# Kernel optimization log

Hardware: AMD Instinct MI355X
Metric: run time of the kernel (lower is better)

The kernel has to match this reference:

```python
import jax, jax.numpy as jnp
import numpy as np

EPS = 1e-5

def setup_inputs() -> dict:
    key = jax.random.key(0)
    k1, k2, k3, k4, k5 = jax.random.split(key, 5)
    B, N, K, HW, C = 2, 128, 64, 65536, 134
    # class probabilities (rows need not be normalized for the matcher math)
    input_class_prob = jax.random.uniform(k1, (B, N, C), dtype=jnp.float32)
    # predicted mask probabilities in [0, 1]
    input_mask = jax.random.uniform(k2, (B, N, HW), dtype=jnp.float32)
    # binary ground-truth masks (stored as float32 for the reduction math)
    target_mask = (jax.random.uniform(k3, (B, K, HW)) > 0.7).astype(jnp.float32)
    target_class = jax.random.randint(k4, (B, K), 0, C, dtype=jnp.int64)
    target_sizes = jax.random.randint(k5, (B,), 1, K + 1, dtype=jnp.int64)
    return {
        "input_class_prob": input_class_prob,
        "input_mask": input_mask,
        "target_mask": target_mask,
        "target_class": target_class,
        "target_sizes": target_sizes,
    }


def reference(input_class_prob, input_mask, target_mask, target_class, target_sizes):
    """Similarity-matrix stage of HungarianMatcher.

    Returns sim: (B, N, K) = sim_class * sim_dice.
    The subsequent scipy linear_sum_assignment is CPU-only with
    data-dependent shapes and is excluded from the kernelizable math.
    """
    B, N, _ = input_class_prob.shape
    K = target_class.shape[-1]
    # sim_class[b, n, k] = input_class_prob[b, n, target_class[b, k]]
    idx = jnp.broadcast_to(target_class[:, None, :], (B, N, K))
    sim_class = jnp.take_along_axis(input_class_prob, idx, axis=-1)
    # dice similarity without materializing the (B, N, K, HW) broadcast:
    # intersections via GEMM, cardinalities via row/col sums + broadcast.
    intersections = jnp.einsum("bnp,bkp->bnk", input_mask, target_mask)
    cardinalities = input_mask.sum(-1)[:, :, None] + target_mask.sum(-1)[:, None, :]
    sim_dice = (2.0 * intersections + EPS) / (cardinalities + EPS)
    return sim_class * sim_dice
```

## Files before the change

### kernel.cpp

```cpp
#include <hip/hip_runtime.h>

#define HWX 65536
#define NQ 128
#define KT 64
#define CC 134
#define BB 2
#define NW 256
#define WIN 256
#define SUB 64
#define NSUB 4
#define EPSI 1e-5f

typedef __attribute__((ext_vector_type(4))) float f32x4;
typedef __attribute__((ext_vector_type(8))) short bf16x8;
typedef __attribute__((ext_vector_type(2))) unsigned int u32x2;

static __device__ __forceinline__ unsigned int cvtpk(float lo, float hi) {
  unsigned int r;
  asm("v_cvt_pk_bf16_f32 %0, %1, %2" : "=v"(r) : "v"(lo), "v"(hi));
  return r;
}

__global__ void hm_detect(const unsigned int* __restrict__ t,
                          unsigned int* __restrict__ flag) {
  unsigned int w = t[threadIdx.x * 2 + 1];
  unsigned long long any = __ballot(w != 0u);
  if (threadIdx.x == 0) *flag = (any != 0ull) ? 1u : 0u;
}

template <bool ATOMIC>
__global__ __launch_bounds__(512, 4)
void hm_stage1(const float* __restrict__ in_mask, const float* __restrict__ tg_mask,
               float* __restrict__ Ipart, float* __restrict__ RSin,
               float* __restrict__ RStg) {
  const int w = blockIdx.x & (NW - 1);
  const int b = blockIdx.x >> 8;
  const int tid = threadIdx.x;
  const int lane = tid & 63;
  const int wv = tid >> 6;
  const int srow = tid >> 4;
  const int c4 = (tid & 15) * 4;
  const int c8b = (tid & 15) * 8;
  const int l16 = lane & 15;
  const int lg = lane >> 4;

  __shared__ unsigned short lA[2][128 * 64];
  __shared__ unsigned short lB[2][64 * 64];

  const float* Ab = in_mask + (size_t)b * NQ * HWX + (size_t)w * WIN;
  const float* Bb = tg_mask + (size_t)b * KT * HWX + (size_t)w * WIN;

  f32x4 ra4[4], rb4[2];
  f32x4 acc[4];
  #pragma unroll
  for (int i = 0; i < 4; ++i) acc[i] = f32x4{0.f, 0.f, 0.f, 0.f};
  float rsA[4] = {0.f, 0.f, 0.f, 0.f};
  float rsB[2] = {0.f, 0.f};

  auto ISSUE = [&](int t) {
    const int co = t * SUB + c4;
    #pragma unroll
    for (int it = 0; it < 4; ++it)
      ra4[it] = *(const f32x4*)(Ab + (size_t)(it * 32 + srow) * HWX + co);
    #pragma unroll
    for (int it = 0; it < 2; ++it)
      rb4[it] = *(const f32x4*)(Bb + (size_t)(it * 32 + srow) * HWX + co);
  };

  auto CVTW = [&](int buf) {
    char* A8 = (char*)lA[buf];
    char* B8 = (char*)lB[buf];
    #pragma unroll
    for (int it = 0; it < 4; ++it) {
      f32x4 x = ra4[it];
      rsA[it] += (x.x + x.y) + (x.z + x.w);
      u32x2 v;
      v.x = cvtpk(x.x, x.y); v.y = cvtpk(x.z, x.w);
      const int row = it * 32 + srow;
      *(u32x2*)(A8 + ((row * 128 + c8b) ^ ((row & 7) << 4))) = v;
    }
    #pragma unroll
    for (int it = 0; it < 2; ++it) {
      f32x4 x = rb4[it];
      rsB[it] += (x.x + x.y) + (x.z + x.w);
      u32x2 v;
      v.x = cvtpk(x.x, x.y); v.y = cvtpk(x.z, x.w);
      const int row = it * 32 + srow;
      *(u32x2*)(B8 + ((row * 128 + c8b) ^ ((row & 7) << 4))) = v;
    }
  };

  auto COMP = [&](int buf) {
    const char* A8 = (const char*)lA[buf];
    const char* B8 = (const char*)lB[buf];
    const int arow = wv * 16 + l16;
    const int sw = (l16 & 7) << 4;
    #pragma unroll
    for (int s = 0; s < 2; ++s) {
      bf16x8 fa = *(const bf16x8*)(A8 + ((arow * 128 + s * 64 + lg * 16) ^ sw));
      #pragma unroll
      for (int cf = 0; cf < 4; ++cf) {
        const int brow = cf * 16 + l16;
        bf16x8 fb = *(const bf16x8*)(B8 + ((brow * 128 + s * 64 + lg * 16) ^ sw));
        acc[cf] = __builtin_amdgcn_mfma_f32_16x16x32_bf16(fa, fb, acc[cf], 0, 0, 0);
      }
    }
  };

  ISSUE(0);
  CVTW(0);
  __syncthreads();
  #pragma unroll
  for (int t = 0; t < NSUB; ++t) {
    if (t + 1 < NSUB) ISSUE(t + 1);
    COMP(t & 1);
    if (t + 1 < NSUB) {
      CVTW((t + 1) & 1);
      __syncthreads();
    }
  }

  #pragma unroll
  for (int cf = 0; cf < 4; ++cf) {
    #pragma unroll
    for (int j = 0; j < 4; ++j) {
      const int row = wv * 16 + lg * 4 + j;
      const int col = cf * 16 + l16;
      if (!ATOMIC)
        Ipart[((size_t)(b * NW + w) * NQ + row) * KT + col] = acc[cf][j];
      else
        atomicAdd(&Ipart[((size_t)b * NQ + row) * KT + col], acc[cf][j]);
    }
  }

  #pragma unroll
  for (int it = 0; it < 4; ++it) {
    float v = rsA[it];
    v += __shfl_xor(v, 1); v += __shfl_xor(v, 2);
    v += __shfl_xor(v, 4); v += __shfl_xor(v, 8);
    rsA[it] = v;
  }
  #pragma unroll
  for (int it = 0; it < 2; ++it) {
    float v = rsB[it];
    v += __shfl_xor(v, 1); v += __shfl_xor(v, 2);
    v += __shfl_xor(v, 4); v += __shfl_xor(v, 8);
    rsB[it] = v;
  }
  if ((tid & 15) == 0) {
    if (!ATOMIC) {
      #pragma unroll
      for (int it = 0; it < 4; ++it)
        RSin[(size_t)(b * NW + w) * NQ + it * 32 + srow] = rsA[it];
      #pragma unroll
      for (int it = 0; it < 2; ++it)
        RStg[(size_t)(b * NW + w) * KT + it * 32 + srow] = rsB[it];
    } else {
      #pragma unroll
      for (int it = 0; it < 4; ++it)
        atomicAdd(&RSin[b * NQ + it * 32 + srow], rsA[it]);
      #pragma unroll
      for (int it = 0; it < 2; ++it)
        atomicAdd(&RStg[b * KT + it * 32 + srow], rsB[it]);
    }
  }
}

__global__ __launch_bounds__(256)
void hm_stage2(const float* __restrict__ cprob, const void* __restrict__ tcls,
               const float* __restrict__ Ipart, const float* __restrict__ RSin,
               const float* __restrict__ RStg, float* __restrict__ out) {
  const int bn = blockIdx.x;
  const int b = bn >> 7, n = bn & 127;
  const int k = threadIdx.x & 63;
  const int wq = threadIdx.x >> 6;
  float I = 0.f, ra = 0.f, rg = 0.f;
  #pragma unroll 8
  for (int ww = 0; ww < NW / 4; ++ww) {
    const int w = wq * (NW / 4) + ww;
    I  += Ipart[((size_t)(b * NW + w) * NQ + n) * KT + k];
    ra += RSin[(size_t)(b * NW + w) * NQ + n];
    rg += RStg[(size_t)(b * NW + w) * KT + k];
  }
  __shared__ float sI[4][64];
  __shared__ float sG[4][64];
  __shared__ float sR[4];
  sI[wq][k] = I;
  sG[wq][k] = rg;
  if (k == 0) sR[wq] = ra;
  __syncthreads();
  if (wq == 0) {
    I  = sI[0][k] + sI[1][k] + sI[2][k] + sI[3][k];
    rg = sG[0][k] + sG[1][k] + sG[2][k] + sG[3][k];
    ra = sR[0] + sR[1] + sR[2] + sR[3];
    const unsigned int hiw = ((const unsigned int*)tcls)[k * 2 + 1];
    const bool i32 = (__ballot(hiw != 0u) != 0ull);
    int tc = i32 ? ((const int*)tcls)[b * KT + k]
                 : (int)((const long long*)tcls)[b * KT + k];
    const float c = cprob[((size_t)b * NQ + n) * CC + tc];
    out[(size_t)bn * KT + k] = c * (2.f * I + EPSI) / (ra + rg + EPSI);
  }
}

__global__ __launch_bounds__(256)
void hm_stage2_direct(const float* __restrict__ cprob, const void* __restrict__ tcls,
                      const unsigned int* __restrict__ flag,
                      const float* __restrict__ Iacc, const float* __restrict__ RSin,
                      const float* __restrict__ RStg, float* __restrict__ out) {
  const int idx = blockIdx.x * 256 + threadIdx.x;
  const int k = idx & 63;
  const int n = (idx >> 6) & 127;
  const int b = idx >> 13;
  const float I  = Iacc[idx];
  const float ra = RSin[b * NQ + n];
  const float rg = RStg[b * KT + k];
  int tc;
  if (*flag) tc = ((const int*)tcls)[b * KT + k];
  else       tc = (int)((const long long*)tcls)[b * KT + k];
  const float c = cprob[((size_t)b * NQ + n) * CC + tc];
  out[idx] = c * (2.f * I + EPSI) / (ra + rg + EPSI);
}

__global__ void hm_zero(float* __restrict__ p, int n) {
  int i = blockIdx.x * blockDim.x + threadIdx.x;
  if (i < n) p[i] = 0.f;
}

extern "C" void kernel_launch(void* const* d_in, const int* in_sizes, int n_in,
                              void* d_out, int out_size, void* d_ws, size_t ws_size,
                              hipStream_t stream) {
  const float* cprob = (const float*)d_in[0];
  const float* imask = (const float*)d_in[1];
  const float* tmask = (const float*)d_in[2];
  const void*  tcls  = d_in[3];
  float* out = (float*)d_out;

  const size_t ipart_f = (size_t)BB * NW * NQ * KT;
  const size_t rsin_f  = (size_t)BB * NW * NQ;
  const size_t rstg_f  = (size_t)BB * NW * KT;
  const size_t need    = (ipart_f + rsin_f + rstg_f) * sizeof(float);

  char* ws = (char*)d_ws;
  if (ws_size >= need) {
    float* Ipart = (float*)ws;
    float* RSin  = Ipart + ipart_f;
    float* RStg  = RSin + rsin_f;
    hm_stage1<false><<<BB * NW, 512, 0, stream>>>(imask, tmask, Ipart, RSin, RStg);
    hm_stage2<<<BB * NQ, 256, 0, stream>>>(cprob, tcls, Ipart, RSin, RStg, out);
  } else {
    float* Iacc = (float*)ws;
    float* RSin = Iacc + (size_t)BB * NQ * KT;
    float* RStg = RSin + BB * NQ;
    unsigned int* flag = (unsigned int*)(RStg + BB * KT);
    const int zn = BB * NQ * KT + BB * NQ + BB * KT;
    hm_zero<<<(zn + 255) / 256, 256, 0, stream>>>(Iacc, zn);
    hm_detect<<<1, 64, 0, stream>>>((const unsigned int*)tcls, flag);
    hm_stage1<true><<<BB * NW, 512, 0, stream>>>(imask, tmask, Iacc, RSin, RStg);
    hm_stage2_direct<<<(BB * NQ * KT) / 256, 256, 0, stream>>>(cprob, tcls, flag, Iacc, RSin, RStg, out);
  }
}
```

Measured before the change: 29.33 us.

## Stage fp32 tiles via direct global-to-LDS loads and convert to bf16 at fragment read

```diff
diff --git a/kernel.cpp b/kernel.cpp
--- a/kernel.cpp
+++ b/kernel.cpp
@@ -5,21 +5,34 @@
 #define KT 64
 #define CC 134
 #define BB 2
-#define NW 256
-#define WIN 256
+#define NW 128
+#define WIN 512
 #define SUB 64
-#define NSUB 4
+#define NSUB 8
 #define EPSI 1e-5f
 
 typedef __attribute__((ext_vector_type(4))) float f32x4;
 typedef __attribute__((ext_vector_type(8))) short bf16x8;
-typedef __attribute__((ext_vector_type(2))) unsigned int u32x2;
+
+union FU { unsigned int u[4]; bf16x8 v; };
 
 static __device__ __forceinline__ unsigned int cvtpk(float lo, float hi) {
   unsigned int r;
   asm("v_cvt_pk_bf16_f32 %0, %1, %2" : "=v"(r) : "v"(lo), "v"(hi));
   return r;
 }
+
+static __device__ __forceinline__ void gload16(const float* g, float* l) {
+  __builtin_amdgcn_global_load_lds(
+      (const __attribute__((address_space(1))) void*)g,
+      (__attribute__((address_space(3))) void*)l, 16, 0, 0);
+}
+
+#define STAGE_SYNC()                                           \
+  do {                                                         \
+    asm volatile("s_waitcnt vmcnt(0)" ::: "memory");           \
+    __syncthreads();                                           \
+  } while (0)
 
 __global__ void hm_detect(const unsigned int* __restrict__ t,
                           unsigned int* __restrict__ flag) {
@@ -29,95 +42,83 @@
 }
 
 template <bool ATOMIC>
-__global__ __launch_bounds__(512, 4)
+__global__ __launch_bounds__(512)
 void hm_stage1(const float* __restrict__ in_mask, const float* __restrict__ tg_mask,
                float* __restrict__ Ipart, float* __restrict__ RSin,
                float* __restrict__ RStg) {
   const int w = blockIdx.x & (NW - 1);
-  const int b = blockIdx.x >> 8;
+  const int b = blockIdx.x >> 7;
   const int tid = threadIdx.x;
   const int lane = tid & 63;
   const int wv = tid >> 6;
-  const int srow = tid >> 4;
-  const int c4 = (tid & 15) * 4;
-  const int c8b = (tid & 15) * 8;
   const int l16 = lane & 15;
   const int lg = lane >> 4;
 
-  __shared__ unsigned short lA[2][128 * 64];
-  __shared__ unsigned short lB[2][64 * 64];
+  __shared__ __align__(16) float lA[2][128 * SUB];
+  __shared__ __align__(16) float lB[2][64 * SUB];
 
   const float* Ab = in_mask + (size_t)b * NQ * HWX + (size_t)w * WIN;
   const float* Bb = tg_mask + (size_t)b * KT * HWX + (size_t)w * WIN;
 
-  f32x4 ra4[4], rb4[2];
   f32x4 acc[4];
   #pragma unroll
   for (int i = 0; i < 4; ++i) acc[i] = f32x4{0.f, 0.f, 0.f, 0.f};
-  float rsA[4] = {0.f, 0.f, 0.f, 0.f};
-  float rsB[2] = {0.f, 0.f};
-
-  auto ISSUE = [&](int t) {
-    const int co = t * SUB + c4;
-    #pragma unroll
-    for (int it = 0; it < 4; ++it)
-      ra4[it] = *(const f32x4*)(Ab + (size_t)(it * 32 + srow) * HWX + co);
-    #pragma unroll
-    for (int it = 0; it < 2; ++it)
-      rb4[it] = *(const f32x4*)(Bb + (size_t)(it * 32 + srow) * HWX + co);
+  float rsA = 0.f;
+  float rsB = 0.f;
+
+  auto STAGE = [&](int t, int buf) {
+    #pragma unroll
+    for (int q = 0; q < 4; ++q) {
+      const int r0 = wv * 16 + q * 4;
+      const int row = r0 + (lane >> 4);
+      const int csrc = (lane & 15) ^ (row & 7);
+      gload16(Ab + (size_t)row * HWX + t * SUB + csrc * 4, &lA[buf][r0 * SUB]);
+    }
+    #pragma unroll
+    for (int q = 0; q < 2; ++q) {
+      const int r0 = wv * 8 + q * 4;
+      const int row = r0 + (lane >> 4);
+      const int csrc = (lane & 15) ^ (row & 7);
+      gload16(Bb + (size_t)row * HWX + t * SUB + csrc * 4, &lB[buf][r0 * SUB]);
+    }
   };
 
-  auto CVTW = [&](int buf) {
-    char* A8 = (char*)lA[buf];
-    char* B8 = (char*)lB[buf];
-    #pragma unroll
-    for (int it = 0; it < 4; ++it) {
-      f32x4 x = ra4[it];
-      rsA[it] += (x.x + x.y) + (x.z + x.w);
-      u32x2 v;
-      v.x = cvtpk(x.x, x.y); v.y = cvtpk(x.z, x.w);
-      const int row = it * 32 + srow;
-      *(u32x2*)(A8 + ((row * 128 + c8b) ^ ((row & 7) << 4))) = v;
-    }
-    #pragma unroll
-    for (int it = 0; it < 2; ++it) {
-      f32x4 x = rb4[it];
-      rsB[it] += (x.x + x.y) + (x.z + x.w);
-      u32x2 v;
-      v.x = cvtpk(x.x, x.y); v.y = cvtpk(x.z, x.w);
-      const int row = it * 32 + srow;
-      *(u32x2*)(B8 + ((row * 128 + c8b) ^ ((row & 7) << 4))) = v;
-    }
-  };
-
   auto COMP = [&](int buf) {
-    const char* A8 = (const char*)lA[buf];
-    const char* B8 = (const char*)lB[buf];
-    const int arow = wv * 16 + l16;
-    const int sw = (l16 & 7) << 4;
+    const float* A32 = lA[buf];
+    const float* B32 = lB[buf];
+    const int xA = l16 & 7;
+    const int Ra = wv * 16 + l16;
     #pragma unroll
     for (int s = 0; s < 2; ++s) {
-      bf16x8 fa = *(const bf16x8*)(A8 + ((arow * 128 + s * 64 + lg * 16) ^ sw));
+      const int g0 = s * 8 + lg * 2;
+      f32x4 alo = *(const f32x4*)(A32 + Ra * SUB + ((g0 ^ xA) << 2));
+      f32x4 ahi = *(const f32x4*)(A32 + Ra * SUB + (((g0 + 1) ^ xA) << 2));
+      rsA += (alo.x + alo.y) + (alo.z + alo.w) + (ahi.x + ahi.y) + (ahi.z + ahi.w);
+      FU fa;
+      fa.u[0] = cvtpk(alo.x, alo.y); fa.u[1] = cvtpk(alo.z, alo.w);
+      fa.u[2] = cvtpk(ahi.x, ahi.y); fa.u[3] = cvtpk(ahi.z, ahi.w);
       #pragma unroll
       for (int cf = 0; cf < 4; ++cf) {
-        const int brow = cf * 16 + l16;
-        bf16x8 fb = *(const bf16x8*)(B8 + ((brow * 128 + s * 64 + lg * 16) ^ sw));
-        acc[cf] = __builtin_amdgcn_mfma_f32_16x16x32_bf16(fa, fb, acc[cf], 0, 0, 0);
+        const int Rb = cf * 16 + l16;
+        f32x4 blo = *(const f32x4*)(B32 + Rb * SUB + ((g0 ^ xA) << 2));
+        f32x4 bhi = *(const f32x4*)(B32 + Rb * SUB + (((g0 + 1) ^ xA) << 2));
+        if (cf == wv)
+          rsB += (blo.x + blo.y) + (blo.z + blo.w) + (bhi.x + bhi.y) + (bhi.z + bhi.w);
+        FU fb;
+        fb.u[0] = cvtpk(blo.x, blo.y); fb.u[1] = cvtpk(blo.z, blo.w);
+        fb.u[2] = cvtpk(bhi.x, bhi.y); fb.u[3] = cvtpk(bhi.z, bhi.w);
+        acc[cf] = __builtin_amdgcn_mfma_f32_16x16x32_bf16(fa.v, fb.v, acc[cf], 0, 0, 0);
       }
     }
   };
 
-  ISSUE(0);
-  CVTW(0);
-  __syncthreads();
+  STAGE(0, 0);
+  STAGE_SYNC();
   #pragma unroll
   for (int t = 0; t < NSUB; ++t) {
-    if (t + 1 < NSUB) ISSUE(t + 1);
+    if (t + 1 < NSUB) STAGE(t + 1, (t + 1) & 1);
     COMP(t & 1);
-    if (t + 1 < NSUB) {
-      CVTW((t + 1) & 1);
-      __syncthreads();
-    }
+    STAGE_SYNC();
   }
 
   #pragma unroll
@@ -133,35 +134,15 @@
     }
   }
 
-  #pragma unroll
-  for (int it = 0; it < 4; ++it) {
-    float v = rsA[it];
-    v += __shfl_xor(v, 1); v += __shfl_xor(v, 2);
-    v += __shfl_xor(v, 4); v += __shfl_xor(v, 8);
-    rsA[it] = v;
-  }
-  #pragma unroll
-  for (int it = 0; it < 2; ++it) {
-    float v = rsB[it];
-    v += __shfl_xor(v, 1); v += __shfl_xor(v, 2);
-    v += __shfl_xor(v, 4); v += __shfl_xor(v, 8);
-    rsB[it] = v;
-  }
-  if ((tid & 15) == 0) {
-    if (!ATOMIC) {
-      #pragma unroll
-      for (int it = 0; it < 4; ++it)
-        RSin[(size_t)(b * NW + w) * NQ + it * 32 + srow] = rsA[it];
-      #pragma unroll
-      for (int it = 0; it < 2; ++it)
-        RStg[(size_t)(b * NW + w) * KT + it * 32 + srow] = rsB[it];
-    } else {
-      #pragma unroll
-      for (int it = 0; it < 4; ++it)
-        atomicAdd(&RSin[b * NQ + it * 32 + srow], rsA[it]);
-      #pragma unroll
-      for (int it = 0; it < 2; ++it)
-        atomicAdd(&RStg[b * KT + it * 32 + srow], rsB[it]);
+  rsA += __shfl_xor(rsA, 16); rsA += __shfl_xor(rsA, 32);
+  rsB += __shfl_xor(rsB, 16); rsB += __shfl_xor(rsB, 32);
+  if (lg == 0) {
+    const int row = wv * 16 + l16;
+    if (!ATOMIC) RSin[(size_t)(b * NW + w) * NQ + row] = rsA;
+    else         atomicAdd(&RSin[b * NQ + row], rsA);
+    if (wv < 4) {
+      if (!ATOMIC) RStg[(size_t)(b * NW + w) * KT + row] = rsB;
+      else         atomicAdd(&RStg[b * KT + row], rsB);
     }
   }
 }
```

Result: faster. 27.82 us (-5.2%).
